# Kernel optimization log

Hardware: AMD Instinct MI355X
Metric: run time of the kernel (lower is better)

The kernel has to match this reference:

```python
import jax, jax.numpy as jnp
import numpy as np

HIDDEN = 512
STATE = 256
DT = 0.1
LN_EPS = 1e-5


def setup_inputs() -> dict:
    key = jax.random.key(0)
    ks = jax.random.split(key, 9)
    B, T = 128, 256
    x = jax.random.normal(ks[0], (B, T, HIDDEN), dtype=jnp.float32)
    A = jax.random.normal(ks[1], (STATE, STATE), dtype=jnp.float32) * 0.01
    # nn.Linear default init scale ~ 1/sqrt(fan_in); exact dist irrelevant for a baseline
    Wb = jax.random.normal(ks[2], (STATE, HIDDEN), dtype=jnp.float32) / np.sqrt(HIDDEN)
    bb = jax.random.normal(ks[3], (STATE,), dtype=jnp.float32) * 0.01
    Wc = jax.random.normal(ks[4], (HIDDEN, STATE), dtype=jnp.float32) / np.sqrt(STATE)
    bc = jax.random.normal(ks[5], (HIDDEN,), dtype=jnp.float32) * 0.01
    Wd = jax.random.normal(ks[6], (HIDDEN, HIDDEN), dtype=jnp.float32) / np.sqrt(HIDDEN)
    bd = jax.random.normal(ks[7], (HIDDEN,), dtype=jnp.float32) * 0.01
    gamma = jnp.ones((HIDDEN,), dtype=jnp.float32)
    beta = jnp.zeros((HIDDEN,), dtype=jnp.float32)
    return {"x": x, "A": A, "Wb": Wb, "bb": bb, "Wc": Wc, "bc": bc,
            "Wd": Wd, "bd": bd, "gamma": gamma, "beta": beta}


def reference(x, A, Wb, bb, Wc, bc, Wd, bd, gamma, beta):
    B, T, H = x.shape
    # discrete transition via matrix exponential (torch.matrix_exp equivalent)
    Ad = jax.scipy.linalg.expm(A * DT)  # [S, S]
    # precompute input injection B(x_t) for all timesteps: [B, T, S]
    Bx = jnp.einsum('bth,sh->bts', x, Wb) + bb
    # linear recurrence h_t = h_{t-1} @ Ad^T + Bx_t via scan over time
    def step(h, bx_t):
        h = h @ Ad.T + bx_t  # [B, S]
        return h, h
    h0 = jnp.zeros((B, STATE), dtype=x.dtype)
    _, hs = jax.lax.scan(step, h0, jnp.swapaxes(Bx, 0, 1))  # hs: [T, B, S]
    hs = jnp.swapaxes(hs, 0, 1)  # [B, T, S]
    # y_t = C(h_t) + D(x_t), vectorized over time
    y = jnp.einsum('bts,hs->bth', hs, Wc) + bc \
        + jnp.einsum('bth,gh->btg', x, Wd) + bd
    # residual + layer norm (dropout is identity in eval mode)
    out = y + x
    mu = jnp.mean(out, axis=-1, keepdims=True)
    var = jnp.var(out, axis=-1, keepdims=True)
    return (out - mu) * jax.lax.rsqrt(var + LN_EPS) * gamma + beta
```

## Files before the change

### kernel.cpp

```cpp
#include <hip/hip_runtime.h>

#define HID 512
#define ST  256
#define BB  128
#define TT  256
#define BT  (BB*TT)
#define NCH 8
#define CHL 32

typedef unsigned short u16;
typedef unsigned int   u32;
typedef float f32x4  __attribute__((ext_vector_type(4)));
typedef __bf16 bf16x8 __attribute__((ext_vector_type(8)));

#define OFF_E    0x0u
#define OFF_EL   0x20000u
#define OFF_W32  0x40000u
#define OFF_WB   0x80000u
#define OFF_WCD  0xC0000u
#define OFF_BIAS 0x180000u
#define OFF_R    0x182000u
#define OFF_HC   0x282000u
#define OFF_U    0x400000u
#define OFF_HS   0x1400000u
#define OFF_XB   0x2400000u

__device__ __forceinline__ u16 f2bf(float f){
  u32 x = __float_as_uint(f);
  return (u16)((x + 0x7FFFu + ((x>>16)&1u)) >> 16);
}
__device__ __forceinline__ float bf2f(u16 u){
  return __uint_as_float(((u32)u)<<16);
}
__device__ __forceinline__ void gld16(const void* g, void* l){
  __builtin_amdgcn_global_load_lds((const __attribute__((address_space(1))) u32*)g,
                                   (__attribute__((address_space(3))) u32*)l, 16, 0, 0);
}

__global__ __launch_bounds__(256) void k_pe(
    const float* __restrict__ x, const float* __restrict__ A,
    const float* __restrict__ Wb, const float* __restrict__ Wc,
    const float* __restrict__ Wd, const float* __restrict__ bc,
    const float* __restrict__ bd, u16* __restrict__ Ebf,
    u16* __restrict__ Elo, u16* __restrict__ wbb,
    u16* __restrict__ wcdb, float* __restrict__ biascd,
    u16* __restrict__ xb)
{
  __shared__ float Ald[32*256];
  __shared__ float cur[256];
  int bid = blockIdx.x;
  int tid = threadIdx.x;
  if (bid < 256){
    int c = tid, lane = tid & 63, w = tid >> 6;
    float a = A[(size_t)bid*256 + c] * 0.1f;
    float s = a;
    cur[c] = a;
    for (int m = 2; m <= 5; ++m){
      float ac0=0.f, ac1=0.f, ac2=0.f, ac3=0.f;
      for (int kb = 0; kb < 256; kb += 32){
        __syncthreads();
        #pragma unroll
        for (int r8 = 0; r8 < 8; ++r8)
          gld16(A + (size_t)kb*256 + r8*1024 + w*256 + lane*4,
                &Ald[r8*1024 + w*256]);
        __syncthreads();
        #pragma unroll
        for (int kk = 0; kk < 32; kk += 4){
          ac0 = fmaf(cur[kb+kk+0], Ald[(kk+0)*256 + c], ac0);
          ac1 = fmaf(cur[kb+kk+1], Ald[(kk+1)*256 + c], ac1);
          ac2 = fmaf(cur[kb+kk+2], Ald[(kk+2)*256 + c], ac2);
          ac3 = fmaf(cur[kb+kk+3], Ald[(kk+3)*256 + c], ac3);
        }
      }
      float n = ((ac0+ac1)+(ac2+ac3)) * (0.1f/(float)m);
      s += n;
      __syncthreads();
      cur[c] = n;
    }
    u16 hi = f2bf(s);
    Ebf[(size_t)bid*256 + c] = hi;
    Elo[(size_t)bid*256 + c] = f2bf(s - bf2f(hi));
    return;
  }
  long gt = (long)(bid - 256)*256 + tid;
  const long np = 2048l*256l;
  for (long i = gt; i < (long)BT*HID/4; i += np){
    float4 v = ((const float4*)x)[i];
    u32 lo = (u32)f2bf(v.x) | ((u32)f2bf(v.y)<<16);
    u32 hi = (u32)f2bf(v.z) | ((u32)f2bf(v.w)<<16);
    uint2 q; q.x = lo; q.y = hi;
    ((uint2*)xb)[i] = q;
  }
  for (long i = gt; i < (long)ST*HID; i += np) wbb[i] = f2bf(Wb[i]);
  for (long i = gt; i < 512l*768l; i += np){
    int n = (int)(i/768), k = (int)(i%768);
    float v = (k < 256) ? Wc[n*256 + k] : Wd[n*512 + (k-256)];
    wcdb[i] = f2bf(v);
  }
  for (long i = gt; i < 512; i += np) biascd[i] = bc[i] + bd[i];
}

__global__ __launch_bounds__(256,1) void k_bx(
    const u16* __restrict__ xb, const u16* __restrict__ wb,
    const float* __restrict__ bb, u16* __restrict__ uout)
{
  __shared__ u16 At[2][128*32];
  __shared__ u16 Bt[2][128*32];
  int bid = blockIdx.x;
  int m0 = (bid>>1)*128, n0 = (bid&1)*128;
  int tid = threadIdx.x, lane = tid&63, w = tid>>6, l15 = lane&15, lg = lane>>4;
  int wrow = (w>>1)*64, wcol = (w&1)*64;
  f32x4 acc[4][4] = {};

  auto stage = [&](int buf, int ki){
    #pragma unroll
    for (int p=0;p<2;++p){
      int c = w + p*4;
      int grow = c*16 + (lane>>2);
      int gk = ki*32 + (lane&3)*8;
      gld16(xb + (size_t)(m0+grow)*HID + gk, &At[buf][c*512]);
      gld16(wb + (size_t)(n0+grow)*HID + gk, &Bt[buf][c*512]);
    }
  };
  stage(0,0);
  __syncthreads();
  for (int ki=0; ki<16; ++ki){
    int buf = ki&1;
    if (ki < 15) stage(buf^1, ki+1);
    bf16x8 af[4], bfr[4];
    #pragma unroll
    for (int mi=0;mi<4;++mi)
      af[mi] = *(const bf16x8*)&At[buf][(wrow + mi*16 + l15)*32 + lg*8];
    #pragma unroll
    for (int ni=0;ni<4;++ni)
      bfr[ni] = *(const bf16x8*)&Bt[buf][(wcol + ni*16 + l15)*32 + lg*8];
    #pragma unroll
    for (int mi=0;mi<4;++mi)
      #pragma unroll
      for (int ni=0;ni<4;++ni)
        acc[mi][ni] = __builtin_amdgcn_mfma_f32_16x16x32_bf16(af[mi], bfr[ni], acc[mi][ni], 0,0,0);
    __syncthreads();
  }
  float bb4[4];
  #pragma unroll
  for (int ni=0;ni<4;++ni) bb4[ni] = bb[n0 + wcol + ni*16 + l15];
  #pragma unroll
  for (int mi=0;mi<4;++mi)
    #pragma unroll
    for (int ni=0;ni<4;++ni)
      #pragma unroll
      for (int r=0;r<4;++r){
        int row = m0 + wrow + mi*16 + lg*4 + r;
        int col = n0 + wcol + ni*16 + l15;
        uout[(size_t)row*ST + col] = f2bf(acc[mi][ni][r] + bb4[ni]);
      }
}

template<bool WRITE_HS>
__global__ __launch_bounds__(256,1) void k_rec(
    const u16* __restrict__ Ebf, const u16* __restrict__ Elo,
    const u16* __restrict__ ubuf, const float* __restrict__ Hc,
    float* __restrict__ Rbuf, u16* __restrict__ hsb,
    float* __restrict__ W32)
{
  int tid = threadIdx.x, lane = tid&63, w = tid>>6, l15 = lane&15, lg = lane>>4;
  __shared__ u16 hlds[2][16*256];

  if (!WRITE_HS && blockIdx.x >= 64){
    int b0 = ((int)blockIdx.x - 64)*16;
    bf16x8 ef[4][8], ef2[4][8];
    #pragma unroll
    for (int nt=0; nt<4; ++nt){
      int srow = w*64 + nt*16 + l15;
      #pragma unroll
      for (int kk=0; kk<8; ++kk){
        ef [nt][kk] = *(const bf16x8*)(Ebf + (size_t)srow*256 + kk*32 + lg*8);
        ef2[nt][kk] = *(const bf16x8*)(Elo + (size_t)srow*256 + kk*32 + lg*8);
      }
    }
    f32x4 acc[4];
    #pragma unroll
    for (int nt=0;nt<4;++nt)
      #pragma unroll
      for (int r=0;r<4;++r)
        acc[nt][r] = (b0 + lg*4 + r == w*64 + nt*16 + l15) ? 1.f : 0.f;
    for (int it=0; it<CHL; ++it){
      u16* hb = hlds[it&1];
      #pragma unroll
      for (int nt=0;nt<4;++nt)
        #pragma unroll
        for (int r=0;r<4;++r){
          int row = lg*4 + r;
          int sc  = w*64 + nt*16 + l15;
          int off = (row*512 + sc*2) ^ ((row&7)<<4);
          hb[off>>1] = f2bf(acc[nt][r]);
        }
      __syncthreads();
      bf16x8 af[8];
      #pragma unroll
      for (int kk=0;kk<8;++kk){
        int off = (l15*512 + (kk*32 + lg*8)*2) ^ ((l15&7)<<4);
        af[kk] = *(const bf16x8*)(hb + (off>>1));
      }
      #pragma unroll
      for (int nt=0;nt<4;++nt)
        #pragma unroll
        for (int kk=0;kk<8;++kk)
          acc[nt] = __builtin_amdgcn_mfma_f32_16x16x32_bf16(af[kk], ef[nt][kk], acc[nt], 0,0,0);
      #pragma unroll
      for (int nt=0;nt<4;++nt)
        #pragma unroll
        for (int kk=0;kk<8;++kk)
          acc[nt] = __builtin_amdgcn_mfma_f32_16x16x32_bf16(af[kk], ef2[nt][kk], acc[nt], 0,0,0);
    }
    #pragma unroll
    for (int nt=0;nt<4;++nt)
      #pragma unroll
      for (int r=0;r<4;++r)
        W32[(size_t)(b0 + lg*4 + r)*256 + w*64 + nt*16 + l15] = acc[nt][r];
    return;
  }

  int j = (int)blockIdx.x >> 3;
  int b0 = ((int)blockIdx.x & 7)*16;

  bf16x8 ef[4][8];
  #pragma unroll
  for (int nt=0; nt<4; ++nt){
    int srow = w*64 + nt*16 + l15;
    #pragma unroll
    for (int kk=0; kk<8; ++kk)
      ef[nt][kk] = *(const bf16x8*)(Ebf + (size_t)srow*256 + kk*32 + lg*8);
  }

  f32x4 acc[4];
  #pragma unroll
  for (int nt=0;nt<4;++nt){
    if (WRITE_HS && j > 0){
      #pragma unroll
      for (int r=0;r<4;++r)
        acc[nt][r] = Hc[((size_t)j*BB + b0 + lg*4 + r)*ST + w*64 + nt*16 + l15];
    } else {
      acc[nt] = (f32x4){0.f,0.f,0.f,0.f};
    }
  }

  int t0 = j*CHL;
  float uv[4][4];
  #pragma unroll
  for (int nt=0;nt<4;++nt)
    #pragma unroll
    for (int r=0;r<4;++r)
      uv[nt][r] = bf2f(ubuf[((size_t)(b0 + lg*4 + r)*TT + t0)*ST + w*64 + nt*16 + l15]);

  for (int it=0; it<CHL; ++it){
    int t = t0 + it;
    u16* hb = hlds[it&1];
    #pragma unroll
    for (int nt=0;nt<4;++nt)
      #pragma unroll
      for (int r=0;r<4;++r){
        int row = lg*4 + r;
        int sc  = w*64 + nt*16 + l15;
        int off = (row*512 + sc*2) ^ ((row&7)<<4);
        hb[off>>1] = f2bf(acc[nt][r]);
      }
    __syncthreads();
    float uvn[4][4];
    if (it+1 < CHL){
      #pragma unroll
      for (int nt=0;nt<4;++nt)
        #pragma unroll
        for (int r=0;r<4;++r)
          uvn[nt][r] = bf2f(ubuf[((size_t)(b0 + lg*4 + r)*TT + t + 1)*ST + w*64 + nt*16 + l15]);
    }
    bf16x8 af[8];
    #pragma unroll
    for (int kk=0;kk<8;++kk){
      int off = (l15*512 + (kk*32 + lg*8)*2) ^ ((l15&7)<<4);
      af[kk] = *(const bf16x8*)(hb + (off>>1));
    }
    #pragma unroll
    for (int nt=0;nt<4;++nt)
      #pragma unroll
      for (int kk=0;kk<8;++kk)
        acc[nt] = __builtin_amdgcn_mfma_f32_16x16x32_bf16(af[kk], ef[nt][kk], acc[nt], 0,0,0);
    #pragma unroll
    for (int nt=0;nt<4;++nt)
      #pragma unroll
      for (int r=0;r<4;++r)
        acc[nt][r] += uv[nt][r];
    if (WRITE_HS){
      #pragma unroll
      for (int nt=0;nt<4;++nt)
        #pragma unroll
        for (int r=0;r<4;++r)
          hsb[((size_t)(b0 + lg*4 + r)*TT + t)*ST + w*64 + nt*16 + l15] = f2bf(acc[nt][r]);
    }
    if (it+1 < CHL){
      #pragma unroll
      for (int nt=0;nt<4;++nt)
        #pragma unroll
        for (int r=0;r<4;++r)
          uv[nt][r] = uvn[nt][r];
    }
  }
  if (!WRITE_HS){
    #pragma unroll
    for (int nt=0;nt<4;++nt)
      #pragma unroll
      for (int r=0;r<4;++r)
        Rbuf[((size_t)j*BB + b0 + lg*4 + r)*ST + w*64 + nt*16 + l15] = acc[nt][r];
  }
}

__global__ __launch_bounds__(256) void k_scan(
    const float* __restrict__ W32, const float* __restrict__ Rbuf,
    float* __restrict__ Hc)
{
  int b = blockIdx.x;
  int s = threadIdx.x;
  __shared__ float hp[256];
  float h = Rbuf[(size_t)(0*BB + b)*ST + s];
  Hc[(size_t)(1*BB + b)*ST + s] = h;
  for (int j = 2; j < NCH; ++j){
    hp[s] = h;
    __syncthreads();
    float a = Rbuf[(size_t)((j-1)*BB + b)*ST + s];
    #pragma unroll 4
    for (int k=0;k<256;++k)
      a = fmaf(hp[k], W32[(size_t)k*256 + s], a);
    __syncthreads();
    h = a;
    Hc[(size_t)j*BB*ST + (size_t)b*ST + s] = h;
  }
}

__global__ __launch_bounds__(512,2) void k_out(
    const u16* __restrict__ hsb, const u16* __restrict__ xb,
    const u16* __restrict__ wcd, const float* __restrict__ biascd,
    const float* __restrict__ gamma, const float* __restrict__ beta,
    float* __restrict__ out)
{
  __shared__ u16 At[2][64*32];
  __shared__ u16 Bt[2][512*32];
  __shared__ float redbuf[64][8][2];
  __shared__ float musig[64][2];
  int m0 = blockIdx.x*64;
  int tid = threadIdx.x, lane = tid&63, w = tid>>6, l15 = lane&15, lg = lane>>4;
  f32x4 acc[4][4] = {};

  auto stage = [&](int buf, int ki){
    #pragma unroll
    for (int p=0;p<4;++p){
      int c = w + p*8;
      gld16(wcd + (size_t)(c*16 + (lane>>2))*768 + ki*32 + (lane&3)*8, &Bt[buf][c*512]);
    }
    if (w < 4){
      const u16* g;
      if (ki < 8) g = hsb + (size_t)(m0 + w*16 + (lane>>2))*ST  + ki*32 + (lane&3)*8;
      else        g = xb  + (size_t)(m0 + w*16 + (lane>>2))*HID + (ki-8)*32 + (lane&3)*8;
      gld16(g, &At[buf][w*512]);
    }
  };
  stage(0,0);
  __syncthreads();
  for (int ki=0; ki<24; ++ki){
    int buf = ki&1;
    if (ki < 23) stage(buf^1, ki+1);
    bf16x8 af[4], bfr[4];
    #pragma unroll
    for (int mi=0;mi<4;++mi)
      af[mi] = *(const bf16x8*)&At[buf][(mi*16 + l15)*32 + lg*8];
    #pragma unroll
    for (int ni=0;ni<4;++ni)
      bfr[ni] = *(const bf16x8*)&Bt[buf][(w*64 + ni*16 + l15)*32 + lg*8];
    #pragma unroll
    for (int mi=0;mi<4;++mi)
      #pragma unroll
      for (int ni=0;ni<4;++ni)
        acc[mi][ni] = __builtin_amdgcn_mfma_f32_16x16x32_bf16(af[mi], bfr[ni], acc[mi][ni], 0,0,0);
    __syncthreads();
  }
  float g4[4], b4[4], bias4[4];
  #pragma unroll
  for (int ni=0;ni<4;++ni){
    int col = w*64 + ni*16 + l15;
    g4[ni] = gamma[col]; b4[ni] = beta[col]; bias4[ni] = biascd[col];
  }
  float psum[4][4] = {}, psq[4][4] = {};
  #pragma unroll
  for (int mi=0;mi<4;++mi)
    #pragma unroll
    for (int ni=0;ni<4;++ni)
      #pragma unroll
      for (int r=0;r<4;++r){
        int row = m0 + mi*16 + lg*4 + r;
        int col = w*64 + ni*16 + l15;
        float v = acc[mi][ni][r] + bias4[ni] + bf2f(xb[(size_t)row*HID + col]);
        acc[mi][ni][r] = v;
        psum[mi][r] += v; psq[mi][r] += v*v;
      }
  #pragma unroll
  for (int mi=0;mi<4;++mi)
    #pragma unroll
    for (int r=0;r<4;++r)
      #pragma unroll
      for (int d=1; d<16; d<<=1){
        psum[mi][r] += __shfl_xor(psum[mi][r], d);
        psq[mi][r]  += __shfl_xor(psq[mi][r], d);
      }
  if (l15 == 0){
    #pragma unroll
    for (int mi=0;mi<4;++mi)
      #pragma unroll
      for (int r=0;r<4;++r){
        int rl = mi*16 + lg*4 + r;
        redbuf[rl][w][0] = psum[mi][r];
        redbuf[rl][w][1] = psq[mi][r];
      }
  }
  __syncthreads();
  if (tid < 64){
    float s=0.f, q=0.f;
    #pragma unroll
    for (int wv=0; wv<8; ++wv){ s += redbuf[tid][wv][0]; q += redbuf[tid][wv][1]; }
    float mu = s*(1.f/512.f);
    float var = q*(1.f/512.f) - mu*mu;
    musig[tid][0] = mu;
    musig[tid][1] = rsqrtf(var + 1e-5f);
  }
  __syncthreads();
  #pragma unroll
  for (int mi=0;mi<4;++mi)
    #pragma unroll
    for (int r=0;r<4;++r){
      int rl = mi*16 + lg*4 + r;
      float mu = musig[rl][0], rs = musig[rl][1];
      #pragma unroll
      for (int ni=0;ni<4;++ni){
        int col = w*64 + ni*16 + l15;
        out[(size_t)(m0+rl)*HID + col] = (acc[mi][ni][r] - mu)*rs*g4[ni] + b4[ni];
      }
    }
}

extern "C" void kernel_launch(void* const* d_in, const int* in_sizes, int n_in,
                              void* d_out, int out_size, void* d_ws, size_t ws_size,
                              hipStream_t stream)
{
  const float* x     = (const float*)d_in[0];
  const float* A     = (const float*)d_in[1];
  const float* Wb    = (const float*)d_in[2];
  const float* bb    = (const float*)d_in[3];
  const float* Wc    = (const float*)d_in[4];
  const float* bc    = (const float*)d_in[5];
  const float* Wd    = (const float*)d_in[6];
  const float* bd    = (const float*)d_in[7];
  const float* gamma = (const float*)d_in[8];
  const float* beta  = (const float*)d_in[9];

  char* ws = (char*)d_ws;
  u16*   Ebf    = (u16*)  (ws + OFF_E);
  u16*   Elo    = (u16*)  (ws + OFF_EL);
  float* W32    = (float*)(ws + OFF_W32);
  u16*   wbb    = (u16*)  (ws + OFF_WB);
  u16*   wcdb   = (u16*)  (ws + OFF_WCD);
  float* biascd = (float*)(ws + OFF_BIAS);
  float* Rbuf   = (float*)(ws + OFF_R);
  float* Hc     = (float*)(ws + OFF_HC);
  u16*   ubuf   = (u16*)  (ws + OFF_U);
  u16*   hsb    = (u16*)  (ws + OFF_HS);
  u16*   xb     = (u16*)  (ws + OFF_XB);

  k_pe<<<2304, 256, 0, stream>>>(x, A, Wb, Wc, Wd, bc, bd, Ebf, Elo, wbb, wcdb, biascd, xb);
  k_bx<<<512, 256, 0, stream>>>(xb, wbb, bb, ubuf);
  k_rec<false><<<80, 256, 0, stream>>>(Ebf, Elo, ubuf, nullptr, Rbuf, nullptr, W32);
  k_scan<<<128, 256, 0, stream>>>(W32, Rbuf, Hc);
  k_rec<true><<<64, 256, 0, stream>>>(Ebf, Elo, ubuf, Hc, nullptr, hsb, W32);
  k_out<<<512, 512, 0, stream>>>(hsb, xb, wcdb, biascd, gamma, beta, (float*)d_out);
}
```

Measured before the change: 384.8 us.

## Compute matrix exponential with MFMA in separate kernel, truncate Taylor to cubic

Moves the expm computation out of the preprocessing kernel into a dedicated 16-block kernel that uses bf16 MFMA with hi/lo split operands. The Taylor series is cut from 5 terms to 3 (M + M^2/2 + M^3/6). Weight transposition loops are also split to avoid div/mod. The goal is to remove the serial scalar FMA matrix-power loop that held 256 blocks in the pre-pass. The cost is lower accuracy in Ad from the truncation and the bf16 M^3 term, plus one extra kernel launch.

```diff
diff --git a/kernel.cpp b/kernel.cpp
--- a/kernel.cpp
+++ b/kernel.cpp
@@ -21,6 +21,8 @@
 #define OFF_BIAS 0x180000u
 #define OFF_R    0x182000u
 #define OFF_HC   0x282000u
+#define OFF_MH   0x390000u
+#define OFF_ML   0x3B0000u
 #define OFF_U    0x400000u
 #define OFF_HS   0x1400000u
 #define OFF_XB   0x2400000u
@@ -41,48 +43,12 @@
     const float* __restrict__ x, const float* __restrict__ A,
     const float* __restrict__ Wb, const float* __restrict__ Wc,
     const float* __restrict__ Wd, const float* __restrict__ bc,
-    const float* __restrict__ bd, u16* __restrict__ Ebf,
-    u16* __restrict__ Elo, u16* __restrict__ wbb,
+    const float* __restrict__ bd, u16* __restrict__ Mhi,
+    u16* __restrict__ Mlo, u16* __restrict__ wbb,
     u16* __restrict__ wcdb, float* __restrict__ biascd,
     u16* __restrict__ xb)
 {
-  __shared__ float Ald[32*256];
-  __shared__ float cur[256];
-  int bid = blockIdx.x;
-  int tid = threadIdx.x;
-  if (bid < 256){
-    int c = tid, lane = tid & 63, w = tid >> 6;
-    float a = A[(size_t)bid*256 + c] * 0.1f;
-    float s = a;
-    cur[c] = a;
-    for (int m = 2; m <= 5; ++m){
-      float ac0=0.f, ac1=0.f, ac2=0.f, ac3=0.f;
-      for (int kb = 0; kb < 256; kb += 32){
-        __syncthreads();
-        #pragma unroll
-        for (int r8 = 0; r8 < 8; ++r8)
-          gld16(A + (size_t)kb*256 + r8*1024 + w*256 + lane*4,
-                &Ald[r8*1024 + w*256]);
-        __syncthreads();
-        #pragma unroll
-        for (int kk = 0; kk < 32; kk += 4){
-          ac0 = fmaf(cur[kb+kk+0], Ald[(kk+0)*256 + c], ac0);
-          ac1 = fmaf(cur[kb+kk+1], Ald[(kk+1)*256 + c], ac1);
-          ac2 = fmaf(cur[kb+kk+2], Ald[(kk+2)*256 + c], ac2);
-          ac3 = fmaf(cur[kb+kk+3], Ald[(kk+3)*256 + c], ac3);
-        }
-      }
-      float n = ((ac0+ac1)+(ac2+ac3)) * (0.1f/(float)m);
-      s += n;
-      __syncthreads();
-      cur[c] = n;
-    }
-    u16 hi = f2bf(s);
-    Ebf[(size_t)bid*256 + c] = hi;
-    Elo[(size_t)bid*256 + c] = f2bf(s - bf2f(hi));
-    return;
-  }
-  long gt = (long)(bid - 256)*256 + tid;
+  long gt = (long)blockIdx.x*256 + threadIdx.x;
   const long np = 2048l*256l;
   for (long i = gt; i < (long)BT*HID/4; i += np){
     float4 v = ((const float4*)x)[i];
@@ -92,12 +58,88 @@
     ((uint2*)xb)[i] = q;
   }
   for (long i = gt; i < (long)ST*HID; i += np) wbb[i] = f2bf(Wb[i]);
-  for (long i = gt; i < 512l*768l; i += np){
-    int n = (int)(i/768), k = (int)(i%768);
-    float v = (k < 256) ? Wc[n*256 + k] : Wd[n*512 + (k-256)];
-    wcdb[i] = f2bf(v);
+  for (long i = gt; i < 512l*256l; i += np)
+    wcdb[(size_t)(i>>8)*768 + (i&255)] = f2bf(Wc[i]);
+  for (long i = gt; i < 512l*512l; i += np)
+    wcdb[(size_t)(i>>9)*768 + 256 + (i&511)] = f2bf(Wd[i]);
+  for (long i = gt; i < 256l*256l; i += np){
+    float m = A[i]*0.1f;
+    u16 h = f2bf(m);
+    Mhi[i] = h;
+    Mlo[i] = f2bf(m - bf2f(h));
   }
   for (long i = gt; i < 512; i += np) biascd[i] = bc[i] + bd[i];
+}
+
+__global__ __launch_bounds__(256,1) void k_expm(
+    const float* __restrict__ A, const u16* __restrict__ Mhi,
+    const u16* __restrict__ Mlo, u16* __restrict__ Ebf,
+    u16* __restrict__ Elo)
+{
+  __shared__ u16 V1h[16*256], V1l[16*256], V2h[16*256];
+  int bn = blockIdx.x;
+  int tid = threadIdx.x, lane = tid&63, w = tid>>6, l15 = lane&15, lg = lane>>4;
+  int j = bn*16 + l15;
+  float v1[4][4];
+  #pragma unroll
+  for (int mi=0;mi<4;++mi)
+    #pragma unroll
+    for (int r=0;r<4;++r){
+      int i = w*64 + mi*16 + lg*4 + r;
+      float v = 0.1f * A[(size_t)i*256 + j];
+      v1[mi][r] = v;
+      u16 h = f2bf(v);
+      int off = (l15*512 + i*2) ^ ((l15&7)<<4);
+      V1h[off>>1] = h;
+      V1l[off>>1] = f2bf(v - bf2f(h));
+    }
+  __syncthreads();
+  f32x4 a2[4] = {};
+  #pragma unroll
+  for (int kk=0;kk<8;++kk){
+    int boff = (l15*512 + (kk*32 + lg*8)*2) ^ ((l15&7)<<4);
+    bf16x8 bh = *(const bf16x8*)(V1h + (boff>>1));
+    bf16x8 bl = *(const bf16x8*)(V1l + (boff>>1));
+    #pragma unroll
+    for (int mi=0;mi<4;++mi){
+      size_t ro = (size_t)(w*64 + mi*16 + l15)*256 + kk*32 + lg*8;
+      bf16x8 ah = *(const bf16x8*)(Mhi + ro);
+      bf16x8 al = *(const bf16x8*)(Mlo + ro);
+      a2[mi] = __builtin_amdgcn_mfma_f32_16x16x32_bf16(ah, bh, a2[mi],0,0,0);
+      a2[mi] = __builtin_amdgcn_mfma_f32_16x16x32_bf16(ah, bl, a2[mi],0,0,0);
+      a2[mi] = __builtin_amdgcn_mfma_f32_16x16x32_bf16(al, bh, a2[mi],0,0,0);
+    }
+  }
+  #pragma unroll
+  for (int mi=0;mi<4;++mi)
+    #pragma unroll
+    for (int r=0;r<4;++r){
+      int i = w*64 + mi*16 + lg*4 + r;
+      int off = (l15*512 + i*2) ^ ((l15&7)<<4);
+      V2h[off>>1] = f2bf(a2[mi][r]);
+    }
+  __syncthreads();
+  f32x4 a3[4] = {};
+  #pragma unroll
+  for (int kk=0;kk<8;++kk){
+    int boff = (l15*512 + (kk*32 + lg*8)*2) ^ ((l15&7)<<4);
+    bf16x8 bh = *(const bf16x8*)(V2h + (boff>>1));
+    #pragma unroll
+    for (int mi=0;mi<4;++mi){
+      bf16x8 ah = *(const bf16x8*)(Mhi + (size_t)(w*64 + mi*16 + l15)*256 + kk*32 + lg*8);
+      a3[mi] = __builtin_amdgcn_mfma_f32_16x16x32_bf16(ah, bh, a3[mi],0,0,0);
+    }
+  }
+  #pragma unroll
+  for (int mi=0;mi<4;++mi)
+    #pragma unroll
+    for (int r=0;r<4;++r){
+      int i = w*64 + mi*16 + lg*4 + r;
+      float s = v1[mi][r] + 0.5f*a2[mi][r] + (1.f/6.f)*a3[mi][r];
+      u16 h = f2bf(s);
+      Ebf[(size_t)i*256 + j] = h;
+      Elo[(size_t)i*256 + j] = f2bf(s - bf2f(h));
+    }
 }
 
 __global__ __launch_bounds__(256,1) void k_bx(
@@ -469,11 +511,14 @@
   float* biascd = (float*)(ws + OFF_BIAS);
   float* Rbuf   = (float*)(ws + OFF_R);
   float* Hc     = (float*)(ws + OFF_HC);
+  u16*   Mhi    = (u16*)  (ws + OFF_MH);
+  u16*   Mlo    = (u16*)  (ws + OFF_ML);
   u16*   ubuf   = (u16*)  (ws + OFF_U);
   u16*   hsb    = (u16*)  (ws + OFF_HS);
   u16*   xb     = (u16*)  (ws + OFF_XB);
 
-  k_pe<<<2304, 256, 0, stream>>>(x, A, Wb, Wc, Wd, bc, bd, Ebf, Elo, wbb, wcdb, biascd, xb);
+  k_pe<<<2048, 256, 0, stream>>>(x, A, Wb, Wc, Wd, bc, bd, Mhi, Mlo, wbb, wcdb, biascd, xb);
+  k_expm<<<16, 256, 0, stream>>>(A, Mhi, Mlo, Ebf, Elo);
   k_bx<<<512, 256, 0, stream>>>(xb, wbb, bb, ubuf);
   k_rec<false><<<80, 256, 0, stream>>>(Ebf, Elo, ubuf, nullptr, Rbuf, nullptr, W32);
   k_scan<<<128, 256, 0, stream>>>(W32, Rbuf, Hc);
```

New measurement: 348.0 us. 9.6% less time.
